# Kernel tuning notes

Hardware: AMD Instinct MI355X
Metric: run time of the kernel (lower is better)

The kernel has to match this reference:

```python
import jax, jax.numpy as jnp
import numpy as np

T, B, V, E, H = 70, 80, 33278, 400, 1150


def _params():
    key = jax.random.key(1)
    ks = jax.random.split(key, 16)
    p = lambda k, shape, s=0.05: jax.random.normal(k, shape, jnp.float32) * s
    return {
        "W_emb": jax.random.uniform(ks[0], (V, E), jnp.float32, -0.1, 0.1),
        "fc_b": p(ks[1], (V,)),
        "Wih1": p(ks[2], (4 * H, E)), "Whh1": p(ks[3], (4 * H, H)),
        "bih1": p(ks[4], (4 * H,)), "bhh1": p(ks[5], (4 * H,)),
        "Wih2": p(ks[6], (4 * H, H)), "Whh2": p(ks[7], (4 * H, H)),
        "bih2": p(ks[8], (4 * H,)), "bhh2": p(ks[9], (4 * H,)),
        "Wih3": p(ks[10], (4 * E, H)), "Whh3": p(ks[11], (4 * E, E)),
        "bih3": p(ks[12], (4 * E,)), "bhh3": p(ks[13], (4 * E,)),
    }


def setup_inputs() -> dict:
    key = jax.random.key(0)
    inp = {
        "input": jax.random.randint(key, (T, B), 0, V, dtype=jnp.int32),
        "s1h": jnp.zeros((B, H), jnp.float32), "s1c": jnp.zeros((B, H), jnp.float32),
        "s2h": jnp.zeros((B, H), jnp.float32), "s2c": jnp.zeros((B, H), jnp.float32),
        "s3h": jnp.zeros((B, E), jnp.float32), "s3c": jnp.zeros((B, E), jnp.float32),
    }
    inp.update(_params())
    return inp


def _lstm(x, h0, c0, Wih, Whh, bih, bhh):
    # x: [T, B, in]; PyTorch gate order: i, f, g, o
    xg = jnp.einsum('tbi,gi->tbg', x, Wih) + bih + bhh  # [T, B, 4H]
    hid = Whh.shape[1]
    def step(carry, xg_t):
        h, c = carry
        g = xg_t + h @ Whh.T
        i = jax.nn.sigmoid(g[:, :hid])
        f = jax.nn.sigmoid(g[:, hid:2 * hid])
        gg = jnp.tanh(g[:, 2 * hid:3 * hid])
        o = jax.nn.sigmoid(g[:, 3 * hid:])
        c = f * c + i * gg
        h = o * jnp.tanh(c)
        return (h, c), h
    (hT, cT), hs = jax.lax.scan(step, (h0, c0), xg)
    return hs, hT, cT


def reference(input, s1h, s1c, s2h, s2c, s3h, s3c, W_emb, fc_b,
              Wih1, Whh1, bih1, bhh1, Wih2, Whh2, bih2, bhh2,
              Wih3, Whh3, bih3, bhh3):
    # eval-mode forward (all dropouts inactive; weight-drop is identity)
    word_vec = W_emb[input]                                  # [T, B, E]
    h1, h1T, c1T = _lstm(word_vec, s1h, s1c, Wih1, Whh1, bih1, bhh1)
    h2, h2T, c2T = _lstm(h1, s2h, s2c, Wih2, Whh2, bih2, bhh2)
    h3, h3T, c3T = _lstm(h2, s3h, s3c, Wih3, Whh3, bih3, bhh3)
    scores = h3.reshape(-1, E) @ W_emb.T + fc_b              # [T*B, V] tied GEMM
    return scores, (h1T, c1T), (h2T, c2T), (h3T, c3T)
```

## Files before the change

### kernel.cpp

```cpp
#include <hip/hip_runtime.h>

typedef unsigned short u16;
typedef __attribute__((ext_vector_type(8))) short short8;
typedef __attribute__((ext_vector_type(4))) float f32x4;

#define T_ 70
#define B_ 80
#define V_ 33278
#define E_ 400
#define H_ 1150
#define EP 416
#define HP 1152
#define G1 4600
#define G1P 4608
#define G3 1600
#define VP 33280
#define M_ 5600
#define MP 5632

__device__ __forceinline__ u16 f2bf(float f) {
  unsigned u = __builtin_bit_cast(unsigned, f);
  u = (u + 0x7fffu + ((u >> 16) & 1u)) >> 16;
  return (u16)u;
}

__device__ __forceinline__ void gload16(const void* g, void* l) {
  __builtin_amdgcn_global_load_lds((const __attribute__((address_space(1))) void*)g,
                                   (__attribute__((address_space(3))) void*)l, 16, 0, 0);
}


__global__ void zero_k(float4* p, long n4) {
  long i = (long)blockIdx.x * blockDim.x + threadIdx.x;
  long stride = (long)gridDim.x * blockDim.x;
  float4 z = {0.f, 0.f, 0.f, 0.f};
  for (; i < n4; i += stride) p[i] = z;
}

__global__ void convert_pad(const float* __restrict__ src, u16* __restrict__ dst,
                            int R, int C, int Cp) {
  int c = blockIdx.x * 256 + threadIdx.x;
  int r = blockIdx.y;
  if (c < Cp) {
    float v = (r < R && c < C) ? src[(size_t)r * C + c] : 0.f;
    dst[(size_t)r * Cp + c] = f2bf(v);
  }
}

__global__ void embed_k(const int* __restrict__ ids, const float* __restrict__ We,
                        u16* __restrict__ x) {
  int r = blockIdx.x;
  int tok = ids[r];
  const float* s = We + (size_t)tok * E_;
  u16* d = x + (size_t)r * EP;
  for (int j = threadIdx.x; j < E_; j += 256) d[j] = f2bf(s[j]);
}

__global__ void stinit_k(const float* __restrict__ s, u16* __restrict__ dst, int H, int Kp) {
  int i = blockIdx.x * 256 + threadIdx.x;
  if (i < B_ * Kp) {
    int r = i / Kp, j = i - r * Kp;
    dst[i] = f2bf(j < H ? s[r * H + j] : 0.f);
  }
}

__global__ void cpy_k(float* __restrict__ d, const float* __restrict__ s, int n) {
  int i = blockIdx.x * 256 + threadIdx.x;
  if (i < n) d[i] = s[i];
}

__global__ void badd_k(float* __restrict__ d, const float* __restrict__ a,
                       const float* __restrict__ b, int n) {
  int i = blockIdx.x * 256 + threadIdx.x;
  if (i < n) d[i] = a[i] + b[i];
}

__global__ __launch_bounds__(256) void gemm_bt(
    const u16* __restrict__ A, const u16* __restrict__ B,
    float* __restrict__ C, const float* __restrict__ bias,
    int M, int Nstore, int Kp, long ldc)
{
  __shared__ u16 lA[128 * 32];
  __shared__ u16 lB[128 * 32];
  const int tid = threadIdx.x;
  const int bm = blockIdx.y, bn = blockIdx.x;
  const int KS = Kp >> 5;
  const int wid = tid >> 6, lane = tid & 63;
  const int wm = (wid >> 1) << 6, wn = (wid & 1) << 6;
  const int lr = lane & 15, lk = lane >> 4;
  f32x4 acc[4][4] = {};
  const u16* Ab = A + (size_t)bm * 128 * Kp;
  const u16* Bb = B + (size_t)bn * 128 * Kp;
  const int sr = tid >> 2;
  const int sc = (tid & 3) << 3;
  for (int ks = 0; ks < KS; ++ks) {
    const int k0 = ks << 5;
    gload16(Ab + (size_t)sr * Kp + k0 + sc, &lA[tid * 8]);
    gload16(Ab + (size_t)(sr + 64) * Kp + k0 + sc, &lA[2048 + tid * 8]);
    gload16(Bb + (size_t)sr * Kp + k0 + sc, &lB[tid * 8]);
    gload16(Bb + (size_t)(sr + 64) * Kp + k0 + sc, &lB[2048 + tid * 8]);
    __syncthreads();
    short8 av[4], bv[4];
#pragma unroll
    for (int mi = 0; mi < 4; ++mi)
      av[mi] = *(const short8*)&lA[(wm + mi * 16 + lr) * 32 + lk * 8];
#pragma unroll
    for (int ni = 0; ni < 4; ++ni)
      bv[ni] = *(const short8*)&lB[(wn + ni * 16 + lr) * 32 + lk * 8];
#pragma unroll
    for (int mi = 0; mi < 4; ++mi)
#pragma unroll
      for (int ni = 0; ni < 4; ++ni)
        acc[mi][ni] = __builtin_amdgcn_mfma_f32_16x16x32_bf16(av[mi], bv[ni], acc[mi][ni], 0, 0, 0);
    __syncthreads();
  }
  const int rb = bm * 128 + wm, cb = bn * 128 + wn;
#pragma unroll
  for (int ni = 0; ni < 4; ++ni) {
    const int cn = cb + ni * 16 + lr;
    if (cn >= Nstore) continue;
    const float badd = bias ? bias[cn] : 0.f;
#pragma unroll
    for (int mi = 0; mi < 4; ++mi) {
      const int r0 = rb + mi * 16 + lk * 4;
#pragma unroll
      for (int r = 0; r < 4; ++r) {
        const int rr = r0 + r;
        if (rr < M) C[(size_t)rr * ldc + cn] = acc[mi][ni][r] + badd;
      }
    }
  }
}

struct LayerArgs {
  const float* xg;
  const u16* Wa; const u16* Xa;
  const u16* Wb; const u16* Xb;
  const float* b;
  float* cbuf; float* hstate; u16* hout;
  int ldxg, Kpa, KSa, Kpb, KSb, H, Kp_out, active;
};

__global__ __launch_bounds__(512) void lstm_step3(LayerArgs L0, LayerArgs L1, LayerArgs L2) {
  __shared__ float gl[B_ * 64];
  const int blk = blockIdx.x;
  LayerArgs L; int jblk;
  if (blk < 72)       { L = L0; jblk = blk; }
  else if (blk < 144) { L = L1; jblk = blk - 72; }
  else                { L = L2; jblk = blk - 144; }
  if (!L.active) return;
  const int tid = threadIdx.x;
  const int wid = tid >> 6, lane = tid & 63;
  const int lr = lane & 15, lk = lane >> 4;
  const int j0 = jblk << 4;
  for (int i = tid; i < B_ * 64; i += 512) gl[i] = 0.f;
  __syncthreads();
  const int KSt = L.KSa + L.KSb;
  const int gs0 = (wid * KSt) >> 3, gs1 = ((wid + 1) * KSt) >> 3;
  f32x4 acc[5][4] = {};
  for (int gs = gs0; gs < gs1; ++gs) {
    const u16* Wp; const u16* Xp; int Kp, k0;
    if (gs < L.KSa) { Wp = L.Wa; Xp = L.Xa; Kp = L.Kpa; k0 = gs << 5; }
    else            { Wp = L.Wb; Xp = L.Xb; Kp = L.Kpb; k0 = (gs - L.KSa) << 5; }
    const int kk = k0 + (lk << 3);
    short8 av[5], bv[4];
#pragma unroll
    for (int mf = 0; mf < 5; ++mf)
      av[mf] = *(const short8*)&Xp[(size_t)(mf * 16 + lr) * Kp + kk];
#pragma unroll
    for (int g = 0; g < 4; ++g)
      bv[g] = *(const short8*)&Wp[(size_t)(g * L.H + j0 + lr) * Kp + kk];
#pragma unroll
    for (int mf = 0; mf < 5; ++mf)
#pragma unroll
      for (int g = 0; g < 4; ++g)
        acc[mf][g] = __builtin_amdgcn_mfma_f32_16x16x32_bf16(av[mf], bv[g], acc[mf][g], 0, 0, 0);
  }
#pragma unroll
  for (int mf = 0; mf < 5; ++mf)
#pragma unroll
    for (int g = 0; g < 4; ++g)
#pragma unroll
      for (int r = 0; r < 4; ++r)
        atomicAdd(&gl[(mf * 16 + lk * 4 + r) * 64 + g * 16 + lr], acc[mf][g][r]);
  __syncthreads();
  const int H = L.H;
  for (int i = tid; i < B_ * 16; i += 512) {
    const int row = i >> 4, jj = i & 15, j = j0 + jj;
    if (j < H) {
      const float* xr = L.xg ? L.xg + (size_t)row * L.ldxg : nullptr;
      float vi = gl[row * 64 + jj]      + (xr ? xr[j]         : 0.f) + L.b[j];
      float vf = gl[row * 64 + 16 + jj] + (xr ? xr[H + j]     : 0.f) + L.b[H + j];
      float vg = gl[row * 64 + 32 + jj] + (xr ? xr[2 * H + j] : 0.f) + L.b[2 * H + j];
      float vo = gl[row * 64 + 48 + jj] + (xr ? xr[3 * H + j] : 0.f) + L.b[3 * H + j];
      float si = 1.f / (1.f + __expf(-vi));
      float sf = 1.f / (1.f + __expf(-vf));
      float tg = tanhf(vg);
      float so = 1.f / (1.f + __expf(-vo));
      float c = sf * L.cbuf[row * H + j] + si * tg;
      L.cbuf[row * H + j] = c;
      float h = so * tanhf(c);
      L.hstate[row * H + j] = h;
      L.hout[(size_t)row * L.Kp_out + j] = f2bf(h);
    }
  }
}

__global__ void tail_k(const float* __restrict__ h1, const float* __restrict__ c1,
                       const float* __restrict__ h2, const float* __restrict__ c2,
                       const float* __restrict__ h3, const float* __restrict__ c3,
                       float* __restrict__ out) {
  int i = blockIdx.x * 256 + threadIdx.x;
  const long base = (long)M_ * V_;
  if (i < 92000)       out[base + i] = h1[i];
  else if (i < 184000) out[base + i] = c1[i - 92000];
  else if (i < 276000) out[base + i] = h2[i - 184000];
  else if (i < 368000) out[base + i] = c2[i - 276000];
  else if (i < 400000) out[base + i] = h3[i - 368000];
  else if (i < 432000) out[base + i] = c3[i - 400000];
}


extern "C" void kernel_launch(void* const* d_in, const int* in_sizes, int n_in,
                              void* d_out, int out_size, void* d_ws, size_t ws_size,
                              hipStream_t stream)
{
  const int*   ids  = (const int*)d_in[0];
  const float* s1h  = (const float*)d_in[1];
  const float* s1c  = (const float*)d_in[2];
  const float* s2h  = (const float*)d_in[3];
  const float* s2c  = (const float*)d_in[4];
  const float* s3h  = (const float*)d_in[5];
  const float* s3c  = (const float*)d_in[6];
  const float* Wemb = (const float*)d_in[7];
  const float* fcb  = (const float*)d_in[8];
  const float* Wih1 = (const float*)d_in[9];
  const float* Whh1 = (const float*)d_in[10];
  const float* bih1 = (const float*)d_in[11];
  const float* bhh1 = (const float*)d_in[12];
  const float* Wih2 = (const float*)d_in[13];
  const float* Whh2 = (const float*)d_in[14];
  const float* bih2 = (const float*)d_in[15];
  const float* bhh2 = (const float*)d_in[16];
  const float* Wih3 = (const float*)d_in[17];
  const float* Whh3 = (const float*)d_in[18];
  const float* bih3 = (const float*)d_in[19];
  const float* bhh3 = (const float*)d_in[20];
  float* out = (float*)d_out;

  char* p = (char*)d_ws;
  auto alloc = [&](size_t bytes) -> char* {
    char* r = p; p += (bytes + 255) & ~(size_t)255; return r;
  };
  u16* WembP = (u16*)alloc((size_t)VP * EP * 2);
  u16* Wih1P = (u16*)alloc((size_t)G1P * EP * 2);
  u16* Whh1P = (u16*)alloc((size_t)G1P * HP * 2);
  u16* Wih2P = (u16*)alloc((size_t)G1P * HP * 2);
  u16* Whh2P = (u16*)alloc((size_t)G1P * HP * 2);
  u16* Wih3P = (u16*)alloc((size_t)G3 * HP * 2);
  u16* Whh3P = (u16*)alloc((size_t)G3 * EP * 2);
  char* zs = p;
  u16* xb  = (u16*)alloc((size_t)MP * EP * 2);
  u16* h1a = (u16*)alloc((size_t)MP * HP * 2);
  u16* h2a = (u16*)alloc((size_t)MP * HP * 2);
  u16* h3a = (u16*)alloc((size_t)MP * EP * 2);
  u16* h1i = (u16*)alloc((size_t)B_ * HP * 2);
  u16* h2i = (u16*)alloc((size_t)B_ * HP * 2);
  u16* h3i = (u16*)alloc((size_t)B_ * EP * 2);
  char* ze = p;
  float* xg1 = (float*)alloc((size_t)M_ * G1P * 4);
  float* c1  = (float*)alloc((size_t)B_ * H_ * 4);
  float* c2  = (float*)alloc((size_t)B_ * H_ * 4);
  float* c3  = (float*)alloc((size_t)B_ * E_ * 4);
  float* h1s = (float*)alloc((size_t)B_ * H_ * 4);
  float* h2s = (float*)alloc((size_t)B_ * H_ * 4);
  float* h3s = (float*)alloc((size_t)B_ * E_ * 4);
  float* b1  = (float*)alloc((size_t)G1 * 4);
  float* b2  = (float*)alloc((size_t)G1 * 4);
  float* b3  = (float*)alloc((size_t)G3 * 4);
  (void)ws_size; (void)in_sizes; (void)n_in; (void)out_size;

  long zn4 = (long)((ze - zs) >> 4);
  zero_k<<<dim3(2048), dim3(256), 0, stream>>>((float4*)zs, zn4);

  convert_pad<<<dim3(2, VP), dim3(256), 0, stream>>>(Wemb, WembP, V_, E_, EP);
  convert_pad<<<dim3(2, G1P), dim3(256), 0, stream>>>(Wih1, Wih1P, G1, E_, EP);
  convert_pad<<<dim3(5, G1P), dim3(256), 0, stream>>>(Whh1, Whh1P, G1, H_, HP);
  convert_pad<<<dim3(5, G1P), dim3(256), 0, stream>>>(Wih2, Wih2P, G1, H_, HP);
  convert_pad<<<dim3(5, G1P), dim3(256), 0, stream>>>(Whh2, Whh2P, G1, H_, HP);
  convert_pad<<<dim3(5, G3), dim3(256), 0, stream>>>(Wih3, Wih3P, G3, H_, HP);
  convert_pad<<<dim3(2, G3), dim3(256), 0, stream>>>(Whh3, Whh3P, G3, E_, EP);

  embed_k<<<dim3(M_), dim3(256), 0, stream>>>(ids, Wemb, xb);
  stinit_k<<<dim3(360), dim3(256), 0, stream>>>(s1h, h1i, H_, HP);
  stinit_k<<<dim3(360), dim3(256), 0, stream>>>(s2h, h2i, H_, HP);
  stinit_k<<<dim3(130), dim3(256), 0, stream>>>(s3h, h3i, E_, EP);
  cpy_k<<<dim3(360), dim3(256), 0, stream>>>(c1, s1c, B_ * H_);
  cpy_k<<<dim3(360), dim3(256), 0, stream>>>(c2, s2c, B_ * H_);
  cpy_k<<<dim3(125), dim3(256), 0, stream>>>(c3, s3c, B_ * E_);
  badd_k<<<dim3(18), dim3(256), 0, stream>>>(b1, bih1, bhh1, G1);
  badd_k<<<dim3(18), dim3(256), 0, stream>>>(b2, bih2, bhh2, G1);
  badd_k<<<dim3(7), dim3(256), 0, stream>>>(b3, bih3, bhh3, G3);

  gemm_bt<<<dim3(G1P / 128, MP / 128), dim3(256), 0, stream>>>(
      xb, Wih1P, xg1, nullptr, M_, G1P, EP, G1P);

  for (int s = 0; s < 72; ++s) {
    LayerArgs L0 = {}, L1 = {}, L2 = {};
    if (s < 70) {
      int t = s;
      L0.active = 1; L0.xg = xg1 + (size_t)t * B_ * G1P; L0.ldxg = G1P;
      L0.Wa = Whh1P; L0.Xa = t ? h1a + (size_t)(t - 1) * B_ * HP : h1i;
      L0.Kpa = HP; L0.KSa = HP / 32; L0.KSb = 0;
      L0.b = b1; L0.cbuf = c1; L0.hstate = h1s;
      L0.hout = h1a + (size_t)t * B_ * HP; L0.H = H_; L0.Kp_out = HP;
    }
    if (s >= 1 && s <= 70) {
      int t = s - 1;
      L1.active = 1; L1.xg = nullptr;
      L1.Wa = Whh2P; L1.Xa = t ? h2a + (size_t)(t - 1) * B_ * HP : h2i;
      L1.Kpa = HP; L1.KSa = HP / 32;
      L1.Wb = Wih2P; L1.Xb = h1a + (size_t)t * B_ * HP;
      L1.Kpb = HP; L1.KSb = HP / 32;
      L1.b = b2; L1.cbuf = c2; L1.hstate = h2s;
      L1.hout = h2a + (size_t)t * B_ * HP; L1.H = H_; L1.Kp_out = HP;
    }
    if (s >= 2) {
      int t = s - 2;
      L2.active = 1; L2.xg = nullptr;
      L2.Wa = Whh3P; L2.Xa = t ? h3a + (size_t)(t - 1) * B_ * EP : h3i;
      L2.Kpa = EP; L2.KSa = EP / 32;
      L2.Wb = Wih3P; L2.Xb = h2a + (size_t)t * B_ * HP;
      L2.Kpb = HP; L2.KSb = HP / 32;
      L2.b = b3; L2.cbuf = c3; L2.hstate = h3s;
      L2.hout = h3a + (size_t)t * B_ * EP; L2.H = E_; L2.Kp_out = EP;
    }
    lstm_step3<<<dim3(169), dim3(512), 0, stream>>>(L0, L1, L2);
  }

  gemm_bt<<<dim3(VP / 128, MP / 128), dim3(256), 0, stream>>>(
      h3a, WembP, out, fcb, M_, V_, EP, (long)V_);
  tail_k<<<dim3(1688), dim3(256), 0, stream>>>(h1s, c1, h2s, c2, h3s, c3, out);
}
```

Before: 6.862 ms.

## Fuse recurrent steps into one cooperative kernel and stage GEMM epilogue stores

The 72 per-step launches of the three-layer LSTM wavefront are replaced by a single cooperative kernel that loops over steps and uses grid.sync between them, removing launch overhead and the gaps between kernels. The GEMM moves to a 1D grid whose M-tile index varies fastest, so consecutive blocks share a B (weight/embedding) tile. Its epilogue stages accumulators through shared memory and writes bias-added float4 rows for coalesced output stores. The cost is grid-wide barrier latency, extra shared memory and syncs in the epilogue, and a need for all 169 blocks to be co-resident.

New measurement: 7.536 ms. 1.1x slower.

```diff
diff --git a/kernel.cpp b/kernel.cpp
--- a/kernel.cpp
+++ b/kernel.cpp
@@ -1,8 +1,12 @@
 #include <hip/hip_runtime.h>
+#include <hip/hip_cooperative_groups.h>
+
+namespace cg = cooperative_groups;
 
 typedef unsigned short u16;
 typedef __attribute__((ext_vector_type(8))) short short8;
 typedef __attribute__((ext_vector_type(4))) float f32x4;
+typedef float float4a __attribute__((ext_vector_type(4), aligned(4)));
 
 #define T_ 70
 #define B_ 80
@@ -75,19 +79,27 @@
   if (i < n) d[i] = a[i] + b[i];
 }
 
-__global__ __launch_bounds__(256) void gemm_bt(
+__global__ __launch_bounds__(256) void gemm_bt2(
     const u16* __restrict__ A, const u16* __restrict__ B,
     float* __restrict__ C, const float* __restrict__ bias,
-    int M, int Nstore, int Kp, long ldc)
+    int M, int Nstore, int Kp, long ldc, int MT)
 {
   __shared__ u16 lA[128 * 32];
   __shared__ u16 lB[128 * 32];
+  __shared__ float st[2][16][132];
+  __shared__ float bsh[128];
   const int tid = threadIdx.x;
-  const int bm = blockIdx.y, bn = blockIdx.x;
+  const int bid = blockIdx.x;
+  const int bm = bid % MT, bn = bid / MT;
   const int KS = Kp >> 5;
   const int wid = tid >> 6, lane = tid & 63;
-  const int wm = (wid >> 1) << 6, wn = (wid & 1) << 6;
+  const int wq = wid >> 1;
+  const int wm = wq << 6, wn = (wid & 1) << 6;
   const int lr = lane & 15, lk = lane >> 4;
+  if (tid < 128) {
+    int gc = bn * 128 + tid;
+    bsh[tid] = (bias && gc < Nstore) ? bias[gc] : 0.f;
+  }
   f32x4 acc[4][4] = {};
   const u16* Ab = A + (size_t)bm * 128 * Kp;
   const u16* Bb = B + (size_t)bn * 128 * Kp;
@@ -114,95 +126,149 @@
         acc[mi][ni] = __builtin_amdgcn_mfma_f32_16x16x32_bf16(av[mi], bv[ni], acc[mi][ni], 0, 0, 0);
     __syncthreads();
   }
-  const int rb = bm * 128 + wm, cb = bn * 128 + wn;
-#pragma unroll
-  for (int ni = 0; ni < 4; ++ni) {
-    const int cn = cb + ni * 16 + lr;
-    if (cn >= Nstore) continue;
-    const float badd = bias ? bias[cn] : 0.f;
-#pragma unroll
-    for (int mi = 0; mi < 4; ++mi) {
-      const int r0 = rb + mi * 16 + lk * 4;
-#pragma unroll
-      for (int r = 0; r < 4; ++r) {
-        const int rr = r0 + r;
-        if (rr < M) C[(size_t)rr * ldc + cn] = acc[mi][ni][r] + badd;
+  const int rgrp = tid >> 7, srow = (tid >> 3) & 15, cq = tid & 7;
+#pragma unroll
+  for (int mi = 0; mi < 4; ++mi) {
+#pragma unroll
+    for (int ni = 0; ni < 4; ++ni)
+#pragma unroll
+      for (int r = 0; r < 4; ++r)
+        st[wq][lk * 4 + r][wn + ni * 16 + lr] = acc[mi][ni][r];
+    __syncthreads();
+    const int gr = bm * 128 + rgrp * 64 + mi * 16 + srow;
+    if (gr < M) {
+      const int gcb = bn * 128 + cq * 16;
+      float* dst = &C[(size_t)gr * ldc + gcb];
+      if (gcb + 15 < Nstore) {
+#pragma unroll
+        for (int q = 0; q < 4; ++q) {
+          float4a v;
+#pragma unroll
+          for (int e = 0; e < 4; ++e)
+            v[e] = st[rgrp][srow][cq * 16 + q * 4 + e] + bsh[cq * 16 + q * 4 + e];
+          *(float4a*)(dst + q * 4) = v;
+        }
+      } else {
+        for (int e = 0; e < 16; ++e)
+          if (gcb + e < Nstore)
+            dst[e] = st[rgrp][srow][cq * 16 + e] + bsh[cq * 16 + e];
       }
     }
-  }
-}
-
-struct LayerArgs {
-  const float* xg;
-  const u16* Wa; const u16* Xa;
-  const u16* Wb; const u16* Xb;
-  const float* b;
-  float* cbuf; float* hstate; u16* hout;
-  int ldxg, Kpa, KSa, Kpb, KSb, H, Kp_out, active;
+    __syncthreads();
+  }
+}
+
+struct RecArgs {
+  const float* xg1;
+  const u16 *Whh1, *Wih2, *Whh2, *Wih3, *Whh3;
+  const u16 *h1i, *h2i, *h3i;
+  u16 *h1a, *h2a, *h3a;
+  const float *b1, *b2, *b3;
+  float *c1, *c2, *c3, *h1s, *h2s, *h3s;
 };
 
-__global__ __launch_bounds__(512) void lstm_step3(LayerArgs L0, LayerArgs L1, LayerArgs L2) {
+__global__ __launch_bounds__(512) void lstm_rec(RecArgs A) {
+  cg::grid_group grid = cg::this_grid();
   __shared__ float gl[B_ * 64];
   const int blk = blockIdx.x;
-  LayerArgs L; int jblk;
-  if (blk < 72)       { L = L0; jblk = blk; }
-  else if (blk < 144) { L = L1; jblk = blk - 72; }
-  else                { L = L2; jblk = blk - 144; }
-  if (!L.active) return;
   const int tid = threadIdx.x;
   const int wid = tid >> 6, lane = tid & 63;
   const int lr = lane & 15, lk = lane >> 4;
+  int layer, jblk;
+  if (blk < 72)       { layer = 0; jblk = blk; }
+  else if (blk < 144) { layer = 1; jblk = blk - 72; }
+  else                { layer = 2; jblk = blk - 144; }
   const int j0 = jblk << 4;
-  for (int i = tid; i < B_ * 64; i += 512) gl[i] = 0.f;
-  __syncthreads();
-  const int KSt = L.KSa + L.KSb;
-  const int gs0 = (wid * KSt) >> 3, gs1 = ((wid + 1) * KSt) >> 3;
-  f32x4 acc[5][4] = {};
-  for (int gs = gs0; gs < gs1; ++gs) {
-    const u16* Wp; const u16* Xp; int Kp, k0;
-    if (gs < L.KSa) { Wp = L.Wa; Xp = L.Xa; Kp = L.Kpa; k0 = gs << 5; }
-    else            { Wp = L.Wb; Xp = L.Xb; Kp = L.Kpb; k0 = (gs - L.KSa) << 5; }
-    const int kk = k0 + (lk << 3);
-    short8 av[5], bv[4];
-#pragma unroll
-    for (int mf = 0; mf < 5; ++mf)
-      av[mf] = *(const short8*)&Xp[(size_t)(mf * 16 + lr) * Kp + kk];
-#pragma unroll
-    for (int g = 0; g < 4; ++g)
-      bv[g] = *(const short8*)&Wp[(size_t)(g * L.H + j0 + lr) * Kp + kk];
-#pragma unroll
-    for (int mf = 0; mf < 5; ++mf)
-#pragma unroll
-      for (int g = 0; g < 4; ++g)
-        acc[mf][g] = __builtin_amdgcn_mfma_f32_16x16x32_bf16(av[mf], bv[g], acc[mf][g], 0, 0, 0);
-  }
-#pragma unroll
-  for (int mf = 0; mf < 5; ++mf)
-#pragma unroll
-    for (int g = 0; g < 4; ++g)
-#pragma unroll
-      for (int r = 0; r < 4; ++r)
-        atomicAdd(&gl[(mf * 16 + lk * 4 + r) * 64 + g * 16 + lr], acc[mf][g][r]);
-  __syncthreads();
-  const int H = L.H;
-  for (int i = tid; i < B_ * 16; i += 512) {
-    const int row = i >> 4, jj = i & 15, j = j0 + jj;
-    if (j < H) {
-      const float* xr = L.xg ? L.xg + (size_t)row * L.ldxg : nullptr;
-      float vi = gl[row * 64 + jj]      + (xr ? xr[j]         : 0.f) + L.b[j];
-      float vf = gl[row * 64 + 16 + jj] + (xr ? xr[H + j]     : 0.f) + L.b[H + j];
-      float vg = gl[row * 64 + 32 + jj] + (xr ? xr[2 * H + j] : 0.f) + L.b[2 * H + j];
-      float vo = gl[row * 64 + 48 + jj] + (xr ? xr[3 * H + j] : 0.f) + L.b[3 * H + j];
-      float si = 1.f / (1.f + __expf(-vi));
-      float sf = 1.f / (1.f + __expf(-vf));
-      float tg = tanhf(vg);
-      float so = 1.f / (1.f + __expf(-vo));
-      float c = sf * L.cbuf[row * H + j] + si * tg;
-      L.cbuf[row * H + j] = c;
-      float h = so * tanhf(c);
-      L.hstate[row * H + j] = h;
-      L.hout[(size_t)row * L.Kp_out + j] = f2bf(h);
+
+  for (int s = 0; s < 72; ++s) {
+    int t; bool active;
+    const u16 *Wa = nullptr, *Xa = nullptr, *Wb = nullptr, *Xb = nullptr;
+    const float *xg = nullptr, *bb = nullptr;
+    float *cb_ = nullptr, *hs_ = nullptr; u16* ho_ = nullptr;
+    int Kpa = 0, KSa = 0, Kpb = 0, KSb = 0, H = 0, Kpo = 0;
+    if (layer == 0) {
+      t = s; active = (t < T_);
+      if (active) {
+        xg = A.xg1 + (size_t)t * B_ * G1P;
+        Wa = A.Whh1; Xa = t ? A.h1a + (size_t)(t - 1) * B_ * HP : A.h1i;
+        Kpa = HP; KSa = HP / 32; KSb = 0;
+        bb = A.b1; cb_ = A.c1; hs_ = A.h1s;
+        ho_ = A.h1a + (size_t)t * B_ * HP; H = H_; Kpo = HP;
+      }
+    } else if (layer == 1) {
+      t = s - 1; active = (s >= 1 && t < T_);
+      if (active) {
+        Wa = A.Whh2; Xa = t ? A.h2a + (size_t)(t - 1) * B_ * HP : A.h2i;
+        Kpa = HP; KSa = HP / 32;
+        Wb = A.Wih2; Xb = A.h1a + (size_t)t * B_ * HP;
+        Kpb = HP; KSb = HP / 32;
+        bb = A.b2; cb_ = A.c2; hs_ = A.h2s;
+        ho_ = A.h2a + (size_t)t * B_ * HP; H = H_; Kpo = HP;
+      }
+    } else {
+      t = s - 2; active = (s >= 2);
+      if (active) {
+        Wa = A.Whh3; Xa = t ? A.h3a + (size_t)(t - 1) * B_ * EP : A.h3i;
+        Kpa = EP; KSa = EP / 32;
+        Wb = A.Wih3; Xb = A.h2a + (size_t)t * B_ * HP;
+        Kpb = HP; KSb = HP / 32;
+        bb = A.b3; cb_ = A.c3; hs_ = A.h3s;
+        ho_ = A.h3a + (size_t)t * B_ * EP; H = E_; Kpo = EP;
+      }
     }
+    if (active) {
+      for (int i = tid; i < B_ * 64; i += 512) gl[i] = 0.f;
+      __syncthreads();
+      const int KSt = KSa + KSb;
+      const int gs0 = (wid * KSt) >> 3, gs1 = ((wid + 1) * KSt) >> 3;
+      f32x4 acc[5][4] = {};
+      for (int gs = gs0; gs < gs1; ++gs) {
+        const u16* Wp; const u16* Xp; int Kp, k0;
+        if (gs < KSa) { Wp = Wa; Xp = Xa; Kp = Kpa; k0 = gs << 5; }
+        else          { Wp = Wb; Xp = Xb; Kp = Kpb; k0 = (gs - KSa) << 5; }
+        const int kk = k0 + (lk << 3);
+        short8 av[5], bv[4];
+#pragma unroll
+        for (int mf = 0; mf < 5; ++mf)
+          av[mf] = *(const short8*)&Xp[(size_t)(mf * 16 + lr) * Kp + kk];
+#pragma unroll
+        for (int g = 0; g < 4; ++g)
+          bv[g] = *(const short8*)&Wp[(size_t)(g * H + j0 + lr) * Kp + kk];
+#pragma unroll
+        for (int mf = 0; mf < 5; ++mf)
+#pragma unroll
+          for (int g = 0; g < 4; ++g)
+            acc[mf][g] = __builtin_amdgcn_mfma_f32_16x16x32_bf16(av[mf], bv[g], acc[mf][g], 0, 0, 0);
+      }
+#pragma unroll
+      for (int mf = 0; mf < 5; ++mf)
+#pragma unroll
+        for (int g = 0; g < 4; ++g)
+#pragma unroll
+          for (int r = 0; r < 4; ++r)
+            atomicAdd(&gl[(mf * 16 + lk * 4 + r) * 64 + g * 16 + lr], acc[mf][g][r]);
+      __syncthreads();
+      for (int i = tid; i < B_ * 16; i += 512) {
+        const int row = i >> 4, jj = i & 15, j = j0 + jj;
+        if (j < H) {
+          const float* xr = xg ? xg + (size_t)row * G1P : nullptr;
+          float vi = gl[row * 64 + jj]      + (xr ? xr[j]         : 0.f) + bb[j];
+          float vf = gl[row * 64 + 16 + jj] + (xr ? xr[H + j]     : 0.f) + bb[H + j];
+          float vg = gl[row * 64 + 32 + jj] + (xr ? xr[2 * H + j] : 0.f) + bb[2 * H + j];
+          float vo = gl[row * 64 + 48 + jj] + (xr ? xr[3 * H + j] : 0.f) + bb[3 * H + j];
+          float si = 1.f / (1.f + __expf(-vi));
+          float sf = 1.f / (1.f + __expf(-vf));
+          float tg = tanhf(vg);
+          float so = 1.f / (1.f + __expf(-vo));
+          float c = sf * cb_[row * H + j] + si * tg;
+          cb_[row * H + j] = c;
+          float h = so * tanhf(c);
+          hs_[row * H + j] = h;
+          ho_[(size_t)row * Kpo + j] = f2bf(h);
+        }
+      }
+    }
+    grid.sync();
   }
 }
 
@@ -302,43 +368,21 @@
   badd_k<<<dim3(18), dim3(256), 0, stream>>>(b2, bih2, bhh2, G1);
   badd_k<<<dim3(7), dim3(256), 0, stream>>>(b3, bih3, bhh3, G3);
 
-  gemm_bt<<<dim3(G1P / 128, MP / 128), dim3(256), 0, stream>>>(
-      xb, Wih1P, xg1, nullptr, M_, G1P, EP, G1P);
-
-  for (int s = 0; s < 72; ++s) {
-    LayerArgs L0 = {}, L1 = {}, L2 = {};
-    if (s < 70) {
-      int t = s;
-      L0.active = 1; L0.xg = xg1 + (size_t)t * B_ * G1P; L0.ldxg = G1P;
-      L0.Wa = Whh1P; L0.Xa = t ? h1a + (size_t)(t - 1) * B_ * HP : h1i;
-      L0.Kpa = HP; L0.KSa = HP / 32; L0.KSb = 0;
-      L0.b = b1; L0.cbuf = c1; L0.hstate = h1s;
-      L0.hout = h1a + (size_t)t * B_ * HP; L0.H = H_; L0.Kp_out = HP;
-    }
-    if (s >= 1 && s <= 70) {
-      int t = s - 1;
-      L1.active = 1; L1.xg = nullptr;
-      L1.Wa = Whh2P; L1.Xa = t ? h2a + (size_t)(t - 1) * B_ * HP : h2i;
-      L1.Kpa = HP; L1.KSa = HP / 32;
-      L1.Wb = Wih2P; L1.Xb = h1a + (size_t)t * B_ * HP;
-      L1.Kpb = HP; L1.KSb = HP / 32;
-      L1.b = b2; L1.cbuf = c2; L1.hstate = h2s;
-      L1.hout = h2a + (size_t)t * B_ * HP; L1.H = H_; L1.Kp_out = HP;
-    }
-    if (s >= 2) {
-      int t = s - 2;
-      L2.active = 1; L2.xg = nullptr;
-      L2.Wa = Whh3P; L2.Xa = t ? h3a + (size_t)(t - 1) * B_ * EP : h3i;
-      L2.Kpa = EP; L2.KSa = EP / 32;
-      L2.Wb = Wih3P; L2.Xb = h2a + (size_t)t * B_ * HP;
-      L2.Kpb = HP; L2.KSb = HP / 32;
-      L2.b = b3; L2.cbuf = c3; L2.hstate = h3s;
-      L2.hout = h3a + (size_t)t * B_ * EP; L2.H = E_; L2.Kp_out = EP;
-    }
-    lstm_step3<<<dim3(169), dim3(512), 0, stream>>>(L0, L1, L2);
-  }
-
-  gemm_bt<<<dim3(VP / 128, MP / 128), dim3(256), 0, stream>>>(
-      h3a, WembP, out, fcb, M_, V_, EP, (long)V_);
+  gemm_bt2<<<dim3(44 * 36), dim3(256), 0, stream>>>(
+      xb, Wih1P, xg1, nullptr, M_, G1P, EP, (long)G1P, 44);
+
+  RecArgs ra;
+  ra.xg1 = xg1;
+  ra.Whh1 = Whh1P; ra.Wih2 = Wih2P; ra.Whh2 = Whh2P; ra.Wih3 = Wih3P; ra.Whh3 = Whh3P;
+  ra.h1i = h1i; ra.h2i = h2i; ra.h3i = h3i;
+  ra.h1a = h1a; ra.h2a = h2a; ra.h3a = h3a;
+  ra.b1 = b1; ra.b2 = b2; ra.b3 = b3;
+  ra.c1 = c1; ra.c2 = c2; ra.c3 = c3;
+  ra.h1s = h1s; ra.h2s = h2s; ra.h3s = h3s;
+  void* kp[] = { &ra };
+  hipLaunchCooperativeKernel((const void*)lstm_rec, dim3(169), dim3(512), kp, 0, stream);
+
+  gemm_bt2<<<dim3(44 * 260), dim3(256), 0, stream>>>(
+      h3a, WembP, out, fcb, M_, V_, EP, (long)V_, 44);
   tail_k<<<dim3(1688), dim3(256), 0, stream>>>(h1s, c1, h2s, c2, h3s, c3, out);
 }
```
